# Performance work log

Hardware: AMD Instinct MI355X
Metric: run time of the kernel (lower is better)

Reference implementation:

```python
import jax, jax.numpy as jnp
import numpy as np

B, S, D, H = 2, 2048, 1024, 16
DEPTH = D // H


def setup_inputs() -> dict:
    key = jax.random.key(0)
    ks = jax.random.split(key, 12)
    inp = {
        "q": jax.random.normal(ks[0], (B, S, D), jnp.float32),
        "k": jax.random.normal(ks[1], (B, S, D), jnp.float32),
        "v": jax.random.normal(ks[2], (B, S - 1, D), jnp.float32),
        # causal mask for the sliced (S-1, S-1) score grid: 1 where masked out
        "mask": jnp.broadcast_to(
            jnp.triu(jnp.ones((S - 1, S - 1), jnp.float32), k=1), (B, S - 1, S - 1)
        ),
        "Wq": jax.random.normal(ks[3], (D, D), jnp.float32) * 0.02,
        "bq": jnp.zeros((D,), jnp.float32),
        "Wk": jax.random.normal(ks[4], (D, D), jnp.float32) * 0.02,
        "bk": jnp.zeros((D,), jnp.float32),
        "Wv": jax.random.normal(ks[5], (D, D), jnp.float32) * 0.02,
        "bv": jnp.zeros((D,), jnp.float32),
        "Wo": jax.random.normal(ks[6], (D, D), jnp.float32) * 0.02,
        "bo": jnp.zeros((D,), jnp.float32),
    }
    return inp


def _split_heads(x):
    # (B, L, D) -> (B, H, L, depth)
    b, l, _ = x.shape
    return x.reshape(b, l, H, DEPTH).transpose(0, 2, 1, 3)


def reference(q, k, v, mask, Wq, bq, Wk, bk, Wv, bv, Wo, bo):
    qq = q @ Wq + bq            # q_layers[0]
    kk = k @ Wk + bk            # k_layers[0]
    vv = v @ Wv + bv            # wv
    qh, kh, vh = _split_heads(qq), _split_heads(kk), _split_heads(vv)
    # scores: (B, H, S, S) then sliced to (B, H, S-1, S-1) as in the source
    scores = jnp.einsum('bhqd,bhkd->bhqk', qh, kh)[:, :, 1:, :-1]
    scale = 1.0 / jnp.sqrt(jnp.asarray(DEPTH, jnp.float32))
    # original casts to fp64 here; JAX default x64-disabled => computed in fp32
    logits = scores * scale + mask[:, None, :, :] * (-1e9)
    att = jax.nn.softmax(logits, axis=-1)   # (B, H, S-1, S-1)
    ctx = jnp.einsum('bhqk,bhkd->bhqd', att, vh)  # v seq len is S-1
    ctx = ctx.transpose(0, 2, 1, 3).reshape(q.shape[0], -1, D)
    out = ctx @ Wo + bo
    return out, att
```

## Files before the change

kernel.cpp:

```cpp
#include <hip/hip_runtime.h>


typedef __attribute__((ext_vector_type(8))) short bf16x8;
typedef __attribute__((ext_vector_type(4))) float f32x4;

#define MFMA_BF16(A, B, C) __builtin_amdgcn_mfma_f32_16x16x32_bf16(A, B, C, 0, 0, 0)

__device__ __forceinline__ short f2bf(float x) {
    unsigned u = __float_as_uint(x);
    u = u + 0x7FFFu + ((u >> 16) & 1u);
    return (short)(u >> 16);
}
__device__ __forceinline__ float bf2f(short s) {
    return __uint_as_float(((unsigned)(unsigned short)s) << 16);
}
__device__ __forceinline__ int imin(int a, int b) { return a < b ? a : b; }

__device__ __forceinline__ void dma16(const short* g, short* l) {
    __builtin_amdgcn_global_load_lds(
        (const __attribute__((address_space(1))) unsigned int*)g,
        (__attribute__((address_space(3))) unsigned int*)l, 16, 0, 0);
}

__global__ __launch_bounds__(256) void transpose_split_kernel(
    const float* __restrict__ W, short* __restrict__ Thi, short* __restrict__ Tlo) {
    __shared__ float tile[32][33];
    const int tx = threadIdx.x & 31, ty = threadIdx.x >> 5;
    const int k0 = blockIdx.x * 32, n0 = blockIdx.y * 32;
#pragma unroll
    for (int p = 0; p < 4; ++p)
        tile[ty + p * 8][tx] = W[(size_t)(k0 + ty + p * 8) * 1024 + n0 + tx];
    __syncthreads();
#pragma unroll
    for (int p = 0; p < 4; ++p) {
        int n = n0 + ty + p * 8, k = k0 + tx;
        float x = tile[tx][ty + p * 8];
        short h = f2bf(x);
        Thi[(size_t)n * 1024 + k] = h;
        if (Tlo) Tlo[(size_t)n * 1024 + k] = f2bf(x - bf2f(h));
    }
}

__global__ __launch_bounds__(256) void split_kernel(
    const float* __restrict__ X, short* __restrict__ Hi, short* __restrict__ Lo, int n8) {
    int idx = blockIdx.x * 256 + threadIdx.x;
    if (idx >= n8) return;
    float4 x0 = *((const float4*)X + (size_t)idx * 2);
    float4 x1 = *((const float4*)X + (size_t)idx * 2 + 1);
    float xs[8] = {x0.x, x0.y, x0.z, x0.w, x1.x, x1.y, x1.z, x1.w};
    bf16x8 hv, lv;
#pragma unroll
    for (int e = 0; e < 8; ++e) {
        short h = f2bf(xs[e]);
        hv[e] = h;
        lv[e] = f2bf(xs[e] - bf2f(h));
    }
    *(bf16x8*)&Hi[(size_t)idx * 8] = hv;
    if (Lo) *(bf16x8*)&Lo[(size_t)idx * 8] = lv;
}

template <int SPLIT, int OUTMODE>
__global__ __launch_bounds__(256) void gemm_dma(
    const short* __restrict__ Ahg, const short* __restrict__ Alg, int M,
    const short* __restrict__ Bhg, const short* __restrict__ Blg,
    const float* __restrict__ bias, float scale,
    float* __restrict__ Cf, short* __restrict__ Chi, short* __restrict__ Clo) {
    __shared__ __align__(16) short Ah[512 * 8];
    __shared__ __align__(16) short Al[SPLIT ? 512 * 8 : 8];
    __shared__ __align__(16) short Bh[256 * 8];
    __shared__ __align__(16) short Bl[SPLIT ? 256 * 8 : 8];

    const int tid = threadIdx.x;
    const int w = tid >> 6, lane = tid & 63;
    const int quad = lane >> 4, l16 = lane & 15;
    const int m0 = blockIdx.y * 128, n0 = blockIdx.x * 64;
    const int row0 = (w & 1) * 64, col0 = (w >> 1) * 32;

    f32x4 acc[4][2];
#pragma unroll
    for (int mi = 0; mi < 4; ++mi)
#pragma unroll
        for (int ni = 0; ni < 2; ++ni) acc[mi][ni] = (f32x4){0.f, 0.f, 0.f, 0.f};

    const int a_row = tid & 127;
    const int a_gr = imin(m0 + a_row, M - 1);
    const int b_gr = n0 + (tid & 63);
    const int b_c = tid >> 6;

    for (int k0 = 0; k0 < 1024; k0 += 32) {
        __syncthreads();
#pragma unroll
        for (int p = 0; p < 2; ++p) {
            int c = (p * 256 + tid) >> 7;
            const size_t go = (size_t)a_gr * 1024 + k0 + c * 8;
            dma16(Ahg + go, &Ah[(p * 256 + tid) * 8]);
            if (SPLIT) dma16(Alg + go, &Al[(p * 256 + tid) * 8]);
        }
        {
            const size_t go = (size_t)b_gr * 1024 + k0 + b_c * 8;
            dma16(Bhg + go, &Bh[tid * 8]);
            if (SPLIT) dma16(Blg + go, &Bl[tid * 8]);
        }
        __syncthreads();

        bf16x8 af[4], afl[4], bfr[2], bfl[2];
#pragma unroll
        for (int mi = 0; mi < 4; ++mi) {
            int r = row0 + mi * 16 + l16;
            af[mi] = *(const bf16x8*)&Ah[(quad * 128 + r) * 8];
            if (SPLIT) afl[mi] = *(const bf16x8*)&Al[(quad * 128 + r) * 8];
        }
#pragma unroll
        for (int ni = 0; ni < 2; ++ni) {
            int cdx = col0 + ni * 16 + l16;
            bfr[ni] = *(const bf16x8*)&Bh[(quad * 64 + cdx) * 8];
            if (SPLIT) bfl[ni] = *(const bf16x8*)&Bl[(quad * 64 + cdx) * 8];
        }
#pragma unroll
        for (int mi = 0; mi < 4; ++mi)
#pragma unroll
            for (int ni = 0; ni < 2; ++ni) {
                acc[mi][ni] = MFMA_BF16(af[mi], bfr[ni], acc[mi][ni]);
                if (SPLIT) {
                    acc[mi][ni] = MFMA_BF16(af[mi], bfl[ni], acc[mi][ni]);
                    acc[mi][ni] = MFMA_BF16(afl[mi], bfr[ni], acc[mi][ni]);
                }
            }
    }

#pragma unroll
    for (int ni = 0; ni < 2; ++ni) {
        int col = n0 + col0 + ni * 16 + l16;
        float bv = bias[col];
#pragma unroll
        for (int mi = 0; mi < 4; ++mi) {
#pragma unroll
            for (int r = 0; r < 4; ++r) {
                int row = m0 + row0 + mi * 16 + quad * 4 + r;
                if (row < M) {
                    float c = (acc[mi][ni][r] + bv) * scale;
                    size_t off = (size_t)row * 1024 + col;
                    if (OUTMODE == 0) {
                        Cf[off] = c;
                    } else if (OUTMODE == 1) {
                        Chi[off] = f2bf(c);
                    } else {
                        short h = f2bf(c);
                        Chi[off] = h;
                        Clo[off] = f2bf(c - bf2f(h));
                    }
                }
            }
        }
    }
}

__global__ __launch_bounds__(256) void transpose_v_kernel(
    const short* __restrict__ VV, short* __restrict__ VT) {
    __shared__ short t[64][72];
    const int tid = threadIdx.x;
    const int st = blockIdx.x & 31, bh = blockIdx.x >> 5;
    const int b = bh >> 4, h = bh & 15;
    const int s0 = st * 64;
    {
        int seq = s0 + (tid >> 2), d0 = (tid & 3) * 16;
        int seqc = imin(seq, 2046);
        const short* src = VV + ((size_t)(b * 2047 + seqc)) * 1024 + h * 64 + d0;
        bf16x8 v0 = *(const bf16x8*)src;
        bf16x8 v1 = *(const bf16x8*)(src + 8);
        bool ok = (seq <= 2046);
#pragma unroll
        for (int e = 0; e < 8; ++e) {
            t[d0 + e][tid >> 2] = ok ? v0[e] : (short)0;
            t[d0 + 8 + e][tid >> 2] = ok ? v1[e] : (short)0;
        }
    }
    __syncthreads();
    {
        int d = tid >> 2, sc2 = (tid & 3) * 16;
        bf16x8 o0, o1;
#pragma unroll
        for (int e = 0; e < 8; ++e) {
            o0[e] = t[d][sc2 + e];
            o1[e] = t[d][sc2 + 8 + e];
        }
        short* dst = VT + ((size_t)(bh * 64 + d)) * 2048 + s0 + sc2;
        *(bf16x8*)dst = o0;
        *(bf16x8*)(dst + 8) = o1;
    }
}

__global__ __launch_bounds__(256) void attn_kernel(
    const short* __restrict__ QQh, const short* __restrict__ QQl,
    const short* __restrict__ KKh, const short* __restrict__ KKl,
    const short* __restrict__ VT,
    float* __restrict__ att, short* __restrict__ CTX) {
    __shared__ __align__(16) short Kh[512 * 8];
    __shared__ __align__(16) short Kl[512 * 8];
    __shared__ __align__(16) short Vt[512 * 8];
    __shared__ __align__(16) short Ps[4][16 * 72];

    const int tid = threadIdx.x;
    const int w = tid >> 6, lane = tid & 63;
    const int quad = lane >> 4, l16 = lane & 15;
    const int bx = blockIdx.x;
    const int qt = 31 - (bx >> 5);
    const int bh = bx & 31;
    const int h = bh & 15, b = bh >> 4;
    const int i0 = qt * 64;

    const int i_frag = i0 + w * 16 + l16;
    const int qrow = imin(i_frag + 1, 2047);
    const size_t qoff = ((size_t)(b * 2048 + qrow)) * 1024 + h * 64;
    const bf16x8 qh0 = *(const bf16x8*)&QQh[qoff + 0 + quad * 8];
    const bf16x8 qh1 = *(const bf16x8*)&QQh[qoff + 32 + quad * 8];
    const bf16x8 ql0 = *(const bf16x8*)&QQl[qoff + 0 + quad * 8];
    const bf16x8 ql1 = *(const bf16x8*)&QQl[qoff + 32 + quad * 8];

    const int i_max = imin(i0 + 63, 2046);
    const int jt_max = i_max >> 6;
    const int wave_imax = imin(i0 + w * 16 + 15, 2046);
    const int rowbase = i0 + w * 16 + quad * 4;

    const int dma_key = tid & 63;
    const int dma_cc0 = tid >> 6;

    float lsum[4] = {0.f, 0.f, 0.f, 0.f};

    for (int jt = 0; jt <= jt_max; ++jt) {
        const int j0 = jt * 64;
        __syncthreads();
#pragma unroll
        for (int p = 0; p < 2; ++p) {
            int cc = p * 4 + dma_cc0;
            dma16(KKh + ((size_t)(b * 2048 + j0 + dma_key)) * 1024 + h * 64 + cc * 8,
                  &Kh[(p * 256 + tid) * 8]);
        }
        __syncthreads();
        if (j0 <= wave_imax) {
#pragma unroll
            for (int s = 0; s < 4; ++s) {
                f32x4 sc = (f32x4){0.f, 0.f, 0.f, 0.f};
#pragma unroll
                for (int c = 0; c < 2; ++c) {
                    bf16x8 kh = *(const bf16x8*)&Kh[((c * 4 + quad) * 64 + s * 16 + l16) * 8];
                    sc = MFMA_BF16(c ? qh1 : qh0, kh, sc);
                    sc = MFMA_BF16(c ? ql1 : ql0, kh, sc);
                }
                int j = j0 + s * 16 + l16;
#pragma unroll
                for (int r = 0; r < 4; ++r) {
                    int i = rowbase + r;
                    if (j <= i && i <= 2046) lsum[r] += __expf(sc[r]);
                }
            }
        }
    }
#pragma unroll
    for (int m = 1; m < 16; m <<= 1) {
#pragma unroll
        for (int r = 0; r < 4; ++r) lsum[r] += __shfl_xor(lsum[r], m, 64);
    }
    float linv[4];
#pragma unroll
    for (int r = 0; r < 4; ++r) linv[r] = 1.0f / lsum[r];

    f32x4 cacc[4];
#pragma unroll
    for (int t = 0; t < 4; ++t) cacc[t] = (f32x4){0.f, 0.f, 0.f, 0.f};

    for (int jt = 0; jt <= jt_max; ++jt) {
        const int j0 = jt * 64;
        __syncthreads();
#pragma unroll
        for (int p = 0; p < 2; ++p) {
            int cc = p * 4 + dma_cc0;
            const size_t ko = ((size_t)(b * 2048 + j0 + dma_key)) * 1024 + h * 64 + cc * 8;
            dma16(KKh + ko, &Kh[(p * 256 + tid) * 8]);
            dma16(KKl + ko, &Kl[(p * 256 + tid) * 8]);
            dma16(VT + ((size_t)(bh * 64 + dma_key)) * 2048 + j0 + cc * 8,
                  &Vt[(p * 256 + tid) * 8]);
        }
        __syncthreads();
        if (j0 <= wave_imax) {
#pragma unroll
            for (int s = 0; s < 4; ++s) {
                f32x4 sc = (f32x4){0.f, 0.f, 0.f, 0.f};
#pragma unroll
                for (int c = 0; c < 2; ++c) {
                    const int ci = ((c * 4 + quad) * 64 + s * 16 + l16) * 8;
                    bf16x8 kh = *(const bf16x8*)&Kh[ci];
                    bf16x8 kl = *(const bf16x8*)&Kl[ci];
                    bf16x8 ah = c ? qh1 : qh0;
                    bf16x8 al = c ? ql1 : ql0;
                    sc = MFMA_BF16(ah, kh, sc);
                    sc = MFMA_BF16(ah, kl, sc);
                    sc = MFMA_BF16(al, kh, sc);
                }
                int j = j0 + s * 16 + l16;
#pragma unroll
                for (int r = 0; r < 4; ++r) {
                    int i = rowbase + r;
                    bool valid = (j <= i) && (i <= 2046);
                    float p = valid ? __expf(sc[r]) * linv[r] : 0.0f;
                    if (i <= 2046 && j <= 2046)
                        att[((size_t)bh * 2047 + i) * 2047 + j] = p;
                    Ps[w][(quad * 4 + r) * 72 + s * 16 + l16] = f2bf(p);
                }
            }
#pragma unroll
            for (int c = 0; c < 2; ++c) {
                bf16x8 pa = *(const bf16x8*)&Ps[w][l16 * 72 + c * 32 + quad * 8];
#pragma unroll
                for (int t = 0; t < 4; ++t) {
                    bf16x8 vb = *(const bf16x8*)&Vt[((c * 4 + quad) * 64 + t * 16 + l16) * 8];
                    cacc[t] = MFMA_BF16(pa, vb, cacc[t]);
                }
            }
        } else {
#pragma unroll
            for (int s = 0; s < 4; ++s) {
                int j = j0 + s * 16 + l16;
#pragma unroll
                for (int r = 0; r < 4; ++r) {
                    int i = rowbase + r;
                    if (i <= 2046 && j <= 2046)
                        att[((size_t)bh * 2047 + i) * 2047 + j] = 0.0f;
                }
            }
        }
    }

#pragma unroll
    for (int t = 0; t < 4; ++t) {
#pragma unroll
        for (int r = 0; r < 4; ++r) {
            int i = rowbase + r;
            if (i <= 2046)
                CTX[((size_t)(b * 2047 + i)) * 1024 + h * 64 + t * 16 + l16] = f2bf(cacc[t][r]);
        }
    }

    const int js = (jt_max + 1) * 64;
    for (int i = i0; i <= i_max; ++i) {
        float* rowp = att + ((size_t)bh * 2047 + i) * 2047;
        for (int cc2 = js + tid; cc2 < 2047; cc2 += 256) rowp[cc2] = 0.0f;
    }
}

extern "C" void kernel_launch(void* const* d_in, const int* in_sizes, int n_in,
                              void* d_out, int out_size, void* d_ws, size_t ws_size,
                              hipStream_t stream) {
    (void)in_sizes; (void)n_in; (void)out_size; (void)ws_size;
    const float* q  = (const float*)d_in[0];
    const float* k  = (const float*)d_in[1];
    const float* v  = (const float*)d_in[2];
    const float* Wq = (const float*)d_in[4];
    const float* bq = (const float*)d_in[5];
    const float* Wk = (const float*)d_in[6];
    const float* bk = (const float*)d_in[7];
    const float* Wv = (const float*)d_in[8];
    const float* bv = (const float*)d_in[9];
    const float* Wo = (const float*)d_in[10];
    const float* bo = (const float*)d_in[11];

    float* out = (float*)d_out;
    float* att = out + (size_t)2 * 2047 * 1024;

    char* ws = (char*)d_ws;
    size_t off = 0;
    auto alloc = [&](size_t bytes) -> void* {
        void* p = ws + off;
        off += (bytes + 255) & ~(size_t)255;
        return p;
    };
    short* Wqt_h = (short*)alloc((size_t)1024 * 1024 * 2);
    short* Wqt_l = (short*)alloc((size_t)1024 * 1024 * 2);
    short* Wkt_h = (short*)alloc((size_t)1024 * 1024 * 2);
    short* Wkt_l = (short*)alloc((size_t)1024 * 1024 * 2);
    short* Wvt_h = (short*)alloc((size_t)1024 * 1024 * 2);
    short* Wot_h = (short*)alloc((size_t)1024 * 1024 * 2);
    short* Qhi = (short*)alloc((size_t)4096 * 1024 * 2);
    short* Qlo = (short*)alloc((size_t)4096 * 1024 * 2);
    short* Khi = (short*)alloc((size_t)4096 * 1024 * 2);
    short* Klo = (short*)alloc((size_t)4096 * 1024 * 2);
    short* Vbf = (short*)alloc((size_t)4096 * 1024 * 2);
    short* QQh = (short*)alloc((size_t)4096 * 1024 * 2);
    short* QQl = (short*)alloc((size_t)4096 * 1024 * 2);
    short* KKh = (short*)alloc((size_t)4096 * 1024 * 2);
    short* KKl = (short*)alloc((size_t)4096 * 1024 * 2);
    short* VV  = (short*)alloc((size_t)4096 * 1024 * 2);
    short* VT  = (short*)alloc((size_t)2048 * 2048 * 2 * 2);
    short* CTX = (short*)alloc((size_t)4096 * 1024 * 2);

    dim3 tgrid(32, 32);
    transpose_split_kernel<<<tgrid, 256, 0, stream>>>(Wq, Wqt_h, Wqt_l);
    transpose_split_kernel<<<tgrid, 256, 0, stream>>>(Wk, Wkt_h, Wkt_l);
    transpose_split_kernel<<<tgrid, 256, 0, stream>>>(Wv, Wvt_h, nullptr);
    transpose_split_kernel<<<tgrid, 256, 0, stream>>>(Wo, Wot_h, nullptr);

    split_kernel<<<2048, 256, 0, stream>>>(q, Qhi, Qlo, 4096 * 1024 / 8);
    split_kernel<<<2048, 256, 0, stream>>>(k, Khi, Klo, 4096 * 1024 / 8);
    split_kernel<<<2047, 256, 0, stream>>>(v, Vbf, nullptr, 4094 * 1024 / 8);

    dim3 ggrid(16, 32);
    gemm_dma<1, 2><<<ggrid, 256, 0, stream>>>(Qhi, Qlo, 4096, Wqt_h, Wqt_l, bq, 0.125f,
                                              nullptr, QQh, QQl);
    gemm_dma<1, 2><<<ggrid, 256, 0, stream>>>(Khi, Klo, 4096, Wkt_h, Wkt_l, bk, 1.0f,
                                              nullptr, KKh, KKl);
    gemm_dma<0, 1><<<ggrid, 256, 0, stream>>>(Vbf, nullptr, 4094, Wvt_h, nullptr, bv, 1.0f,
                                              nullptr, VV, nullptr);

    transpose_v_kernel<<<dim3(32 * 32), 256, 0, stream>>>(VV, VT);

    attn_kernel<<<dim3(32 * 32), 256, 0, stream>>>(QQh, QQl, KKh, KKl, VT, att, CTX);

    gemm_dma<0, 0><<<ggrid, 256, 0, stream>>>(CTX, nullptr, 4094, Wot_h, nullptr, bo, 1.0f,
                                              out, nullptr, nullptr);
}
```

Measured before the change: 997.9 us.

## Double-buffer attention K/V tiles, fold log2e into Q scale, vectorize att zero-fill

The attention kernel now double-buffers its K and V shared-memory tiles in both passes. The DMA for tile jt+1 is issued before computing tile jt, which leaves one barrier per iteration instead of two and overlaps global loads with MFMA work. Log2(e) is folded into the Q projection scale so the softmax can call the hardware exp2 directly. The tail zero-fill of the att rows switches to aligned float4 stores. Shared memory use doubles, which may lower occupancy.

```diff
diff --git a/kernel.cpp b/kernel.cpp
--- a/kernel.cpp
+++ b/kernel.cpp
@@ -15,6 +15,14 @@
     return __uint_as_float(((unsigned)(unsigned short)s) << 16);
 }
 __device__ __forceinline__ int imin(int a, int b) { return a < b ? a : b; }
+
+__device__ __forceinline__ float fexp2(float x) {
+#if __has_builtin(__builtin_amdgcn_exp2f)
+    return __builtin_amdgcn_exp2f(x);
+#else
+    return __expf(x * 0.69314718055994531f);
+#endif
+}
 
 __device__ __forceinline__ void dma16(const short* g, short* l) {
     __builtin_amdgcn_global_load_lds(
@@ -195,9 +203,9 @@
     const short* __restrict__ KKh, const short* __restrict__ KKl,
     const short* __restrict__ VT,
     float* __restrict__ att, short* __restrict__ CTX) {
-    __shared__ __align__(16) short Kh[512 * 8];
-    __shared__ __align__(16) short Kl[512 * 8];
-    __shared__ __align__(16) short Vt[512 * 8];
+    __shared__ __align__(16) short KH[2][512 * 8];
+    __shared__ __align__(16) short KL[2][512 * 8];
+    __shared__ __align__(16) short VS[2][512 * 8];
     __shared__ __align__(16) short Ps[4][16 * 72];
 
     const int tid = threadIdx.x;
@@ -227,23 +235,41 @@
 
     float lsum[4] = {0.f, 0.f, 0.f, 0.f};
 
-    for (int jt = 0; jt <= jt_max; ++jt) {
-        const int j0 = jt * 64;
-        __syncthreads();
+    auto stageA = [&](int jt, int buf) {
 #pragma unroll
         for (int p = 0; p < 2; ++p) {
             int cc = p * 4 + dma_cc0;
-            dma16(KKh + ((size_t)(b * 2048 + j0 + dma_key)) * 1024 + h * 64 + cc * 8,
-                  &Kh[(p * 256 + tid) * 8]);
-        }
-        __syncthreads();
+            dma16(KKh + ((size_t)(b * 2048 + jt * 64 + dma_key)) * 1024 + h * 64 + cc * 8,
+                  &KH[buf][(p * 256 + tid) * 8]);
+        }
+    };
+    auto stageB = [&](int jt, int buf) {
+#pragma unroll
+        for (int p = 0; p < 2; ++p) {
+            int cc = p * 4 + dma_cc0;
+            const size_t ko =
+                ((size_t)(b * 2048 + jt * 64 + dma_key)) * 1024 + h * 64 + cc * 8;
+            dma16(KKh + ko, &KH[buf][(p * 256 + tid) * 8]);
+            dma16(KKl + ko, &KL[buf][(p * 256 + tid) * 8]);
+            dma16(VT + ((size_t)(bh * 64 + dma_key)) * 2048 + jt * 64 + cc * 8,
+                  &VS[buf][(p * 256 + tid) * 8]);
+        }
+    };
+
+    stageA(0, 0);
+    __syncthreads();
+    int cur = 0;
+    for (int jt = 0; jt <= jt_max; ++jt) {
+        if (jt < jt_max) stageA(jt + 1, cur ^ 1);
+        const int j0 = jt * 64;
         if (j0 <= wave_imax) {
 #pragma unroll
             for (int s = 0; s < 4; ++s) {
                 f32x4 sc = (f32x4){0.f, 0.f, 0.f, 0.f};
 #pragma unroll
                 for (int c = 0; c < 2; ++c) {
-                    bf16x8 kh = *(const bf16x8*)&Kh[((c * 4 + quad) * 64 + s * 16 + l16) * 8];
+                    bf16x8 kh =
+                        *(const bf16x8*)&KH[cur][((c * 4 + quad) * 64 + s * 16 + l16) * 8];
                     sc = MFMA_BF16(c ? qh1 : qh0, kh, sc);
                     sc = MFMA_BF16(c ? ql1 : ql0, kh, sc);
                 }
@@ -251,10 +277,12 @@
 #pragma unroll
                 for (int r = 0; r < 4; ++r) {
                     int i = rowbase + r;
-                    if (j <= i && i <= 2046) lsum[r] += __expf(sc[r]);
-                }
-            }
-        }
+                    if (j <= i && i <= 2046) lsum[r] += fexp2(sc[r]);
+                }
+            }
+        }
+        __syncthreads();
+        cur ^= 1;
     }
 #pragma unroll
     for (int m = 1; m < 16; m <<= 1) {
@@ -269,19 +297,12 @@
 #pragma unroll
     for (int t = 0; t < 4; ++t) cacc[t] = (f32x4){0.f, 0.f, 0.f, 0.f};
 
+    stageB(0, 0);
+    __syncthreads();
+    cur = 0;
     for (int jt = 0; jt <= jt_max; ++jt) {
+        if (jt < jt_max) stageB(jt + 1, cur ^ 1);
         const int j0 = jt * 64;
-        __syncthreads();
-#pragma unroll
-        for (int p = 0; p < 2; ++p) {
-            int cc = p * 4 + dma_cc0;
-            const size_t ko = ((size_t)(b * 2048 + j0 + dma_key)) * 1024 + h * 64 + cc * 8;
-            dma16(KKh + ko, &Kh[(p * 256 + tid) * 8]);
-            dma16(KKl + ko, &Kl[(p * 256 + tid) * 8]);
-            dma16(VT + ((size_t)(bh * 64 + dma_key)) * 2048 + j0 + cc * 8,
-                  &Vt[(p * 256 + tid) * 8]);
-        }
-        __syncthreads();
         if (j0 <= wave_imax) {
 #pragma unroll
             for (int s = 0; s < 4; ++s) {
@@ -289,8 +310,8 @@
 #pragma unroll
                 for (int c = 0; c < 2; ++c) {
                     const int ci = ((c * 4 + quad) * 64 + s * 16 + l16) * 8;
-                    bf16x8 kh = *(const bf16x8*)&Kh[ci];
-                    bf16x8 kl = *(const bf16x8*)&Kl[ci];
+                    bf16x8 kh = *(const bf16x8*)&KH[cur][ci];
+                    bf16x8 kl = *(const bf16x8*)&KL[cur][ci];
                     bf16x8 ah = c ? qh1 : qh0;
                     bf16x8 al = c ? ql1 : ql0;
                     sc = MFMA_BF16(ah, kh, sc);
@@ -302,7 +323,7 @@
                 for (int r = 0; r < 4; ++r) {
                     int i = rowbase + r;
                     bool valid = (j <= i) && (i <= 2046);
-                    float p = valid ? __expf(sc[r]) * linv[r] : 0.0f;
+                    float p = valid ? fexp2(sc[r]) * linv[r] : 0.0f;
                     if (i <= 2046 && j <= 2046)
                         att[((size_t)bh * 2047 + i) * 2047 + j] = p;
                     Ps[w][(quad * 4 + r) * 72 + s * 16 + l16] = f2bf(p);
@@ -313,7 +334,8 @@
                 bf16x8 pa = *(const bf16x8*)&Ps[w][l16 * 72 + c * 32 + quad * 8];
 #pragma unroll
                 for (int t = 0; t < 4; ++t) {
-                    bf16x8 vb = *(const bf16x8*)&Vt[((c * 4 + quad) * 64 + t * 16 + l16) * 8];
+                    bf16x8 vb =
+                        *(const bf16x8*)&VS[cur][((c * 4 + quad) * 64 + t * 16 + l16) * 8];
                     cacc[t] = MFMA_BF16(pa, vb, cacc[t]);
                 }
             }
@@ -329,6 +351,8 @@
                 }
             }
         }
+        __syncthreads();
+        cur ^= 1;
     }
 
 #pragma unroll
@@ -342,9 +366,19 @@
     }
 
     const int js = (jt_max + 1) * 64;
-    for (int i = i0; i <= i_max; ++i) {
-        float* rowp = att + ((size_t)bh * 2047 + i) * 2047;
-        for (int cc2 = js + tid; cc2 < 2047; cc2 += 256) rowp[cc2] = 0.0f;
+    if (js < 2047) {
+        const float4 z4 = {0.f, 0.f, 0.f, 0.f};
+        for (int i = i0; i <= i_max; ++i) {
+            const size_t base = (size_t)(bh * 2047 + i) * 2047;
+            float* rowp = att + base;
+            int aligned = js + (int)((4 - ((base + js) & 3)) & 3);
+            if (aligned > 2047) aligned = 2047;
+            for (int c = js + tid; c < aligned; c += 256) rowp[c] = 0.0f;
+            int nv = (2047 - aligned) >> 2;
+            for (int q = tid; q < nv; q += 256)
+                *(float4*)(rowp + aligned + q * 4) = z4;
+            for (int c = aligned + nv * 4 + tid; c < 2047; c += 256) rowp[c] = 0.0f;
+        }
     }
 }
 
@@ -404,7 +438,8 @@
     split_kernel<<<2047, 256, 0, stream>>>(v, Vbf, nullptr, 4094 * 1024 / 8);
 
     dim3 ggrid(16, 32);
-    gemm_dma<1, 2><<<ggrid, 256, 0, stream>>>(Qhi, Qlo, 4096, Wqt_h, Wqt_l, bq, 0.125f,
+    const float qscale = 0.125f * 1.44269504088896341f;
+    gemm_dma<1, 2><<<ggrid, 256, 0, stream>>>(Qhi, Qlo, 4096, Wqt_h, Wqt_l, bq, qscale,
                                               nullptr, QQh, QQl);
     gemm_dma<1, 2><<<ggrid, 256, 0, stream>>>(Khi, Klo, 4096, Wkt_h, Wkt_l, bk, 1.0f,
                                               nullptr, KKh, KKl);
```

After: 988.5 us. No clear change (-0.9%).
